# Performance work log

Measured on AMD Instinct MI355X. Metric: run time of the kernel, lower is better.

Reference implementation:

```python
import jax, jax.numpy as jnp
import numpy as np

B, T, C, H = 4, 4096, 1024, 64  # batch, seq, n_embd, head_size

def setup_inputs() -> dict:
    key = jax.random.key(0)
    kx, kq, kk, kv = jax.random.split(key, 4)
    x = jax.random.normal(kx, (B, T, C), dtype=jnp.float32)
    s = 1.0 / np.sqrt(C)
    Wq = jax.random.normal(kq, (C, H), dtype=jnp.float32) * s
    Wk = jax.random.normal(kk, (C, H), dtype=jnp.float32) * s
    Wv = jax.random.normal(kv, (C, H), dtype=jnp.float32) * s
    return {"x": x, "Wq": Wq, "Wk": Wk, "Wv": Wv}

def reference(x, Wq, Wk, Wv):
    B_, T_, C_ = x.shape
    q = x @ Wq  # [B,T,H]
    k = x @ Wk
    v = x @ Wv
    # NOTE: original scales by C**-0.5 (n_embd), not head_size**-0.5
    scale = jnp.asarray(C_, x.dtype) ** -0.5
    wei = jnp.einsum('bth,bsh->bts', q, k) * scale  # [B,T,T]
    causal = jnp.tril(jnp.ones((T_, T_), dtype=bool))
    wei = jnp.where(causal, wei, -jnp.inf)
    wei = jax.nn.softmax(wei, axis=-1)
    out = jnp.einsum('bts,bsh->bth', wei, v)  # [B,T,H]
    return out
```

## Files before the change

### kernel.cpp

```cpp
#include <hip/hip_runtime.h>
#include <hip/hip_bf16.h>
#include <math.h>

#define BB 4
#define TT 4096
#define CC 1024
#define HH 64

typedef __attribute__((ext_vector_type(8))) short short8;
typedef __attribute__((ext_vector_type(8))) unsigned short ushort8;
typedef __attribute__((ext_vector_type(4))) float f32x4;
typedef __attribute__((ext_vector_type(2))) unsigned int uint2v;
typedef __attribute__((ext_vector_type(4))) unsigned int uint4v;

__device__ inline unsigned short f2bf(float f) {
    unsigned int u = __builtin_bit_cast(unsigned int, f);
    unsigned int r = u + 0x7fffu + ((u >> 16) & 1u);
    return (unsigned short)(r >> 16);
}

__device__ inline unsigned int cvtpk(float lo, float hi) {
    unsigned int r;
    asm("v_cvt_pk_bf16_f32 %0, %1, %2" : "=v"(r) : "v"(lo), "v"(hi));
    return r;
}

__device__ inline void gll16(const void* g, void* l) {
    __builtin_amdgcn_global_load_lds(
        (const __attribute__((address_space(1))) unsigned int*)g,
        (__attribute__((address_space(3))) unsigned int*)l,
        16, 0, 0);
}

__device__ inline int soff_strip(int qs) {
    if (qs < 128) return (qs - 64) * 2;
    if (qs < 192) return 128 + (qs - 128) * 3;
    return 320 + (qs - 192) * 4;
}

__global__ __launch_bounds__(256) void wtrans_kernel(
    const float* __restrict__ Wq,
    const float* __restrict__ Wk,
    const float* __restrict__ Wv,
    unsigned short* __restrict__ Wf)
{
    const int t = blockIdx.x * 256 + threadIdx.x;
    const int lane = t & 63;
    const int ntl  = (t >> 6) % 12;
    const int kt   = t / 768;
    const int quad = lane >> 4, n = lane & 15;
    const int m    = ntl >> 2;
    const int col  = (ntl & 3) * 16 + n;
    const float* src = (m == 0) ? Wq : (m == 1) ? Wk : Wv;
    ushort8 u;
#pragma unroll
    for (int j = 0; j < 8; ++j)
        u[j] = f2bf(src[(kt * 32 + quad * 8 + j) * 64 + col]);
    *(ushort8*)(Wf + (size_t)t * 8) = u;
}

__global__ __launch_bounds__(512, 2) void qkv_gemm(
    const float* __restrict__ x,
    const unsigned short* __restrict__ Wf,
    unsigned short* __restrict__ Qb,
    unsigned short* __restrict__ Kf,
    unsigned short* __restrict__ Vf)
{
    __shared__ __align__(16) unsigned char smem[81920];
    float (*Tl)[200] = (float (*)[200])smem;

    const int tid  = threadIdx.x;
    const int lane = tid & 63;
    const int wave = tid >> 6;
    const int n    = lane & 15;
    const int quad = lane >> 4;
    const int mt   = wave & 3;
    const int ch   = wave >> 2;

    const int row0g = blockIdx.x * 64;
    const int b     = row0g >> 12;
    const int st    = (row0g & (TT - 1)) >> 6;

    const char* xg = (const char*)(x + (size_t)row0g * CC);
    const char* wg = (const char*)Wf;

    f32x4 acc[6];
#pragma unroll
    for (int i = 0; i < 6; ++i) acc[i] = (f32x4){0.f, 0.f, 0.f, 0.f};

    auto stage = [&](int bb, int s) {
        unsigned char* base = smem + bb * 40960;
#pragma unroll
        for (int i = 0; i < 2; ++i) {
            const int rr = (i * 8 + wave) * 4 + (lane >> 4);
            const int cb = ((lane & 15) * 16) ^ ((rr & 7) << 4);
            gll16(xg + (size_t)rr * 4096 + s * 256 + cb,
                  base + (i * 8 + wave) * 1024);
        }
#pragma unroll
        for (int i = 0; i < 3; ++i) {
            const int off = (i * 8 + wave) * 1024;
            gll16(wg + (size_t)s * 24576 + off + lane * 16,
                  base + 16384 + off);
        }
    };

    auto compute = [&](int bb) {
        const unsigned char* xb = smem + bb * 40960;
        const unsigned char* wb = xb + 16384;
        const int row = mt * 16 + n;
        const int swz = (n & 7) << 4;
#pragma unroll
        for (int ktl = 0; ktl < 2; ++ktl) {
            const int c0 = (ktl * 128 + quad * 32) ^ swz;
            const int c1 = (ktl * 128 + quad * 32 + 16) ^ swz;
            const float4 f0 = *(const float4*)(xb + row * 256 + c0);
            const float4 f1 = *(const float4*)(xb + row * 256 + c1);
            uint4v u;
            u[0] = cvtpk(f0.x, f0.y);
            u[1] = cvtpk(f0.z, f0.w);
            u[2] = cvtpk(f1.x, f1.y);
            u[3] = cvtpk(f1.z, f1.w);
            const short8 a0 = __builtin_bit_cast(short8, u);
#pragma unroll
            for (int t = 0; t < 6; ++t) {
                const int g = ch * 6 + t;
                const short8 bwv = *(const short8*)(wb + (ktl * 12 + g) * 1024 + lane * 16);
                acc[t] = __builtin_amdgcn_mfma_f32_16x16x32_bf16(a0, bwv, acc[t], 0, 0, 0);
            }
        }
    };

    stage(0, 0);
    __syncthreads();
#pragma unroll 2
    for (int s = 0; s < 16; ++s) {
        if (s + 1 < 16) stage((s + 1) & 1, s + 1);
        compute(s & 1);
        __syncthreads();
    }

#pragma unroll
    for (int t = 0; t < 6; ++t) {
        const int g   = ch * 6 + t;
        const int col = (g >> 2) * 64 + (g & 3) * 16 + n;
#pragma unroll
        for (int r = 0; r < 4; ++r)
            Tl[mt * 16 + quad * 4 + r][col] = acc[t][r];
    }
    __syncthreads();

    {
        const int row = tid & 63;
        const int c0  = (tid >> 6) * 8;
        uint4v w4;
        w4[0] = cvtpk(Tl[row][c0]     * 0.03125f, Tl[row][c0 + 1] * 0.03125f);
        w4[1] = cvtpk(Tl[row][c0 + 2] * 0.03125f, Tl[row][c0 + 3] * 0.03125f);
        w4[2] = cvtpk(Tl[row][c0 + 4] * 0.03125f, Tl[row][c0 + 5] * 0.03125f);
        w4[3] = cvtpk(Tl[row][c0 + 6] * 0.03125f, Tl[row][c0 + 7] * 0.03125f);
        *(uint4v*)(Qb + (size_t)(row0g + row) * HH + c0) = w4;
    }
    {
        const int mt2 = wave >> 1, kk = wave & 1;
        ushort8 u;
#pragma unroll
        for (int j = 0; j < 8; ++j)
            u[j] = f2bf(Tl[mt2 * 16 + n][64 + kk * 32 + quad * 8 + j]);
        const size_t r = (size_t)(((b * 64 + st) * 4 + mt2) * 2 + kk) * 64 + lane;
        *(ushort8*)(Kf + r * 8) = u;
    }
    {
        const int ht = wave >> 1, kv = wave & 1;
        ushort8 u;
#pragma unroll
        for (int j = 0; j < 8; ++j)
            u[j] = f2bf(Tl[kv * 32 + quad * 8 + j][128 + ht * 16 + n]);
        const size_t r = (size_t)(((b * 64 + st) * 4 + ht) * 2 + kv) * 64 + lane;
        *(ushort8*)(Vf + r * 8) = u;
    }
}

__global__ __launch_bounds__(256) void attn_kernel(
    const unsigned short* __restrict__ Qb,
    const unsigned short* __restrict__ Kf,
    const unsigned short* __restrict__ Vf,
    float* __restrict__ out,
    float* __restrict__ scr)
{
    __shared__ unsigned short Ps[4][2][16][72];

    const int tid  = threadIdx.x;
    const int lane = tid & 63;
    const int wave = tid >> 6;
    const int n    = lane & 15;
    const int quad = lane >> 4;

    const int wid = blockIdx.x * 4 + wave;
    const int b   = wid / 640;
    const int u   = wid - b * 640;

    int qs, ci;
    if (u < 64)        { qs = u;                  ci = 0; }
    else if (u < 192)  { const int v = u - 64;  qs = 64  + (v >> 1); ci = v & 1; }
    else if (u < 384)  { const int v = u - 192; const int d = v / 3;
                         qs = 128 + d;            ci = v - 3 * d; }
    else               { const int v = u - 384; qs = 192 + (v >> 2); ci = v & 3; }

    const int stmax = qs >> 2;
    const int st0   = ci << 4;
    const int stEnd = min(stmax, st0 + 15);
    const int nc    = (stmax + 16) >> 4;
    const int qrow  = qs * 16 + n;

    const unsigned short* qp = Qb + ((size_t)b * TT + qrow) * HH;
    const short8 bQ0 = *(const short8*)(qp + quad * 8);
    const short8 bQ1 = *(const short8*)(qp + 32 + quad * 8);

    const unsigned short* KfB = Kf + (size_t)b * 262144;
    const unsigned short* VfB = Vf + (size_t)b * 262144;

    f32x4 O[4];
#pragma unroll
    for (int ht = 0; ht < 4; ++ht) O[ht] = (f32x4){0.f, 0.f, 0.f, 0.f};
    float l = 0.f;

    short8 kA[4], kB[4];
#pragma unroll
    for (int mt = 0; mt < 4; ++mt) {
        const unsigned short* kp = KfB + (size_t)((st0 * 4 + mt) * 2) * 512 + lane * 8;
        kA[mt] = *(const short8*)(kp);
        kB[mt] = *(const short8*)(kp + 512);
    }

    for (int st = st0; st <= stEnd; ++st) {
        f32x4 S[4];
#pragma unroll
        for (int mt = 0; mt < 4; ++mt) {
            f32x4 acc = (f32x4){0.f, 0.f, 0.f, 0.f};
            acc = __builtin_amdgcn_mfma_f32_16x16x32_bf16(kA[mt], bQ0, acc, 0, 0, 0);
            acc = __builtin_amdgcn_mfma_f32_16x16x32_bf16(kB[mt], bQ1, acc, 0, 0, 0);
            S[mt] = acc;
        }

        short8 vA[4], vB[4];
#pragma unroll
        for (int ht = 0; ht < 4; ++ht) {
            const unsigned short* vp = VfB + (size_t)((st * 4 + ht) * 2) * 512 + lane * 8;
            vA[ht] = *(const short8*)(vp);
            vB[ht] = *(const short8*)(vp + 512);
        }
        if (st < stEnd) {
#pragma unroll
            for (int mt = 0; mt < 4; ++mt) {
                const unsigned short* kp = KfB + (size_t)(((st + 1) * 4 + mt) * 2) * 512 + lane * 8;
                kA[mt] = *(const short8*)(kp);
                kB[mt] = *(const short8*)(kp + 512);
            }
        }

        if (st == stmax) {
#pragma unroll
            for (int mt = 0; mt < 4; ++mt) {
                const int sg = st * 64 + mt * 16 + quad * 4;
#pragma unroll
                for (int r = 0; r < 4; ++r)
                    if (sg + r > qrow) S[mt][r] = -INFINITY;
            }
        }

#pragma unroll
        for (int mt = 0; mt < 4; ++mt)
#pragma unroll
            for (int r = 0; r < 4; ++r) {
                const float p = __expf(fminf(S[mt][r], 30.f));
                S[mt][r] = p;
                l += p;
            }

        const int pp = st & 1;
#pragma unroll
        for (int mt = 0; mt < 4; ++mt) {
            uint2v w;
            w[0] = (unsigned int)f2bf(S[mt][0]) | ((unsigned int)f2bf(S[mt][1]) << 16);
            w[1] = (unsigned int)f2bf(S[mt][2]) | ((unsigned int)f2bf(S[mt][3]) << 16);
            *(uint2v*)&Ps[wave][pp][n][mt * 16 + quad * 4] = w;
        }
        asm volatile("s_waitcnt lgkmcnt(0)" ::: "memory");
        const short8 bP0 = *(const short8*)&Ps[wave][pp][n][quad * 8];
        const short8 bP1 = *(const short8*)&Ps[wave][pp][n][32 + quad * 8];

#pragma unroll
        for (int ht = 0; ht < 4; ++ht) {
            O[ht] = __builtin_amdgcn_mfma_f32_16x16x32_bf16(vA[ht], bP0, O[ht], 0, 0, 0);
            O[ht] = __builtin_amdgcn_mfma_f32_16x16x32_bf16(vB[ht], bP1, O[ht], 0, 0, 0);
        }
    }

    l += __shfl_xor(l, 16);
    l += __shfl_xor(l, 32);

    if (nc == 1) {
        const float inv = 1.0f / l;
        float* op = out + ((size_t)b * TT + qrow) * HH;
#pragma unroll
        for (int ht = 0; ht < 4; ++ht) {
            float4 o4;
            o4.x = O[ht][0] * inv;
            o4.y = O[ht][1] * inv;
            o4.z = O[ht][2] * inv;
            o4.w = O[ht][3] * inv;
            *(float4*)(op + ht * 16 + quad * 4) = o4;
        }
    } else {
        float* sb = scr + (size_t)(b * 576 + soff_strip(qs) + ci) * 1040;
        float* rp = sb + n * 64;
#pragma unroll
        for (int ht = 0; ht < 4; ++ht)
            *(f32x4*)(rp + ht * 16 + quad * 4) = O[ht];
        if (quad == 0) sb[1024 + n] = l;
    }
}

__global__ __launch_bounds__(64) void combine_kernel(
    const float* __restrict__ scr,
    float* __restrict__ out)
{
    const int b  = blockIdx.x / 192;
    const int qs = 64 + blockIdx.x % 192;
    const int nc = ((qs >> 2) + 16) >> 4;
    const int base = b * 576 + soff_strip(qs);

    const int t    = threadIdx.x;
    const int row  = t >> 2;
    const int col0 = (t & 3) * 16;

    f32x4 s0 = (f32x4){0.f,0.f,0.f,0.f}, s1 = s0, s2 = s0, s3 = s0;
    float lsum = 0.f;
    for (int ci = 0; ci < nc; ++ci) {
        const float* sb = scr + (size_t)(base + ci) * 1040;
        lsum += sb[1024 + row];
        const float* p = sb + row * 64 + col0;
        s0 += *(const f32x4*)(p);
        s1 += *(const f32x4*)(p + 4);
        s2 += *(const f32x4*)(p + 8);
        s3 += *(const f32x4*)(p + 12);
    }
    const float inv = 1.0f / lsum;
    float* op = out + ((size_t)b * TT + qs * 16 + row) * HH + col0;
    *(f32x4*)(op)      = s0 * inv;
    *(f32x4*)(op + 4)  = s1 * inv;
    *(f32x4*)(op + 8)  = s2 * inv;
    *(f32x4*)(op + 12) = s3 * inv;
}

extern "C" void kernel_launch(void* const* d_in, const int* in_sizes, int n_in,
                              void* d_out, int out_size, void* d_ws, size_t ws_size,
                              hipStream_t stream)
{
    const float* x  = (const float*)d_in[0];
    const float* Wq = (const float*)d_in[1];
    const float* Wk = (const float*)d_in[2];
    const float* Wv = (const float*)d_in[3];

    unsigned short* Qb = (unsigned short*)d_ws;
    unsigned short* Wf = Qb + (size_t)BB * TT * HH;
    unsigned short* Kf = Wf + (size_t)192 * 1024;
    unsigned short* Vf = Kf + (size_t)BB * 262144;
    float*          scr = (float*)(Vf + (size_t)BB * 262144);
    float* out = (float*)d_out;

    wtrans_kernel<<<96, 256, 0, stream>>>(Wq, Wk, Wv, Wf);
    qkv_gemm<<<BB * TT / 64, 512, 0, stream>>>(x, Wf, Qb, Kf, Vf);
    attn_kernel<<<640, 256, 0, stream>>>(Qb, Kf, Vf, out, scr);
    combine_kernel<<<768, 64, 0, stream>>>(scr, out);
}
```

Measured before the change: 150.0 us.

## Process two query strips per wave to reuse K/V fragments

```diff
diff --git a/kernel.cpp b/kernel.cpp
--- a/kernel.cpp
+++ b/kernel.cpp
@@ -180,14 +180,14 @@
     }
 }
 
-__global__ __launch_bounds__(256) void attn_kernel(
+__global__ __launch_bounds__(256, 2) void attn_kernel(
     const unsigned short* __restrict__ Qb,
     const unsigned short* __restrict__ Kf,
     const unsigned short* __restrict__ Vf,
     float* __restrict__ out,
     float* __restrict__ scr)
 {
-    __shared__ unsigned short Ps[4][2][16][72];
+    __shared__ unsigned short Ps[4][2][2][16][72];
 
     const int tid  = threadIdx.x;
     const int lane = tid & 63;
@@ -196,33 +196,41 @@
     const int quad = lane >> 4;
 
     const int wid = blockIdx.x * 4 + wave;
-    const int b   = wid / 640;
-    const int u   = wid - b * 640;
-
-    int qs, ci;
-    if (u < 64)        { qs = u;                  ci = 0; }
-    else if (u < 192)  { const int v = u - 64;  qs = 64  + (v >> 1); ci = v & 1; }
-    else if (u < 384)  { const int v = u - 192; const int d = v / 3;
-                         qs = 128 + d;            ci = v - 3 * d; }
-    else               { const int v = u - 384; qs = 192 + (v >> 2); ci = v & 3; }
-
-    const int stmax = qs >> 2;
+    const int b   = wid / 320;
+    const int u   = wid - b * 320;
+
+    int g, ci;
+    if (u < 32)        { g = u;                 ci = 0; }
+    else if (u < 96)   { const int v = u - 32;  g = 32 + (v >> 1); ci = v & 1; }
+    else if (u < 192)  { const int v = u - 96;  const int d = v / 3;
+                         g = 64 + d;            ci = v - 3 * d; }
+    else               { const int v = u - 192; g = 96 + (v >> 2); ci = v & 3; }
+
+    const int qs0   = 2 * g, qs1 = 2 * g + 1;
+    const int stmax = g >> 1;
     const int st0   = ci << 4;
     const int stEnd = min(stmax, st0 + 15);
     const int nc    = (stmax + 16) >> 4;
-    const int qrow  = qs * 16 + n;
-
-    const unsigned short* qp = Qb + ((size_t)b * TT + qrow) * HH;
-    const short8 bQ0 = *(const short8*)(qp + quad * 8);
-    const short8 bQ1 = *(const short8*)(qp + 32 + quad * 8);
+    const int qrow0 = qs0 * 16 + n;
+    const int qrow1 = qrow0 + 16;
+
+    const unsigned short* qp0 = Qb + ((size_t)b * TT + qrow0) * HH;
+    const unsigned short* qp1 = Qb + ((size_t)b * TT + qrow1) * HH;
+    const short8 bQ0a = *(const short8*)(qp0 + quad * 8);
+    const short8 bQ1a = *(const short8*)(qp0 + 32 + quad * 8);
+    const short8 bQ0b = *(const short8*)(qp1 + quad * 8);
+    const short8 bQ1b = *(const short8*)(qp1 + 32 + quad * 8);
 
     const unsigned short* KfB = Kf + (size_t)b * 262144;
     const unsigned short* VfB = Vf + (size_t)b * 262144;
 
-    f32x4 O[4];
-#pragma unroll
-    for (int ht = 0; ht < 4; ++ht) O[ht] = (f32x4){0.f, 0.f, 0.f, 0.f};
-    float l = 0.f;
+    f32x4 Oa[4], Ob[4];
+#pragma unroll
+    for (int ht = 0; ht < 4; ++ht) {
+        Oa[ht] = (f32x4){0.f, 0.f, 0.f, 0.f};
+        Ob[ht] = (f32x4){0.f, 0.f, 0.f, 0.f};
+    }
+    float la = 0.f, lb = 0.f;
 
     short8 kA[4], kB[4];
 #pragma unroll
@@ -233,13 +241,17 @@
     }
 
     for (int st = st0; st <= stEnd; ++st) {
-        f32x4 S[4];
+        f32x4 Sa[4], Sb[4];
 #pragma unroll
         for (int mt = 0; mt < 4; ++mt) {
-            f32x4 acc = (f32x4){0.f, 0.f, 0.f, 0.f};
-            acc = __builtin_amdgcn_mfma_f32_16x16x32_bf16(kA[mt], bQ0, acc, 0, 0, 0);
-            acc = __builtin_amdgcn_mfma_f32_16x16x32_bf16(kB[mt], bQ1, acc, 0, 0, 0);
-            S[mt] = acc;
+            f32x4 a = (f32x4){0.f, 0.f, 0.f, 0.f};
+            a = __builtin_amdgcn_mfma_f32_16x16x32_bf16(kA[mt], bQ0a, a, 0, 0, 0);
+            a = __builtin_amdgcn_mfma_f32_16x16x32_bf16(kB[mt], bQ1a, a, 0, 0, 0);
+            Sa[mt] = a;
+            f32x4 c = (f32x4){0.f, 0.f, 0.f, 0.f};
+            c = __builtin_amdgcn_mfma_f32_16x16x32_bf16(kA[mt], bQ0b, c, 0, 0, 0);
+            c = __builtin_amdgcn_mfma_f32_16x16x32_bf16(kB[mt], bQ1b, c, 0, 0, 0);
+            Sb[mt] = c;
         }
 
         short8 vA[4], vB[4];
@@ -263,8 +275,10 @@
             for (int mt = 0; mt < 4; ++mt) {
                 const int sg = st * 64 + mt * 16 + quad * 4;
 #pragma unroll
-                for (int r = 0; r < 4; ++r)
-                    if (sg + r > qrow) S[mt][r] = -INFINITY;
+                for (int r = 0; r < 4; ++r) {
+                    if (sg + r > qrow0) Sa[mt][r] = -INFINITY;
+                    if (sg + r > qrow1) Sb[mt][r] = -INFINITY;
+                }
             }
         }
 
@@ -272,52 +286,75 @@
         for (int mt = 0; mt < 4; ++mt)
 #pragma unroll
             for (int r = 0; r < 4; ++r) {
-                const float p = __expf(fminf(S[mt][r], 30.f));
-                S[mt][r] = p;
-                l += p;
+                const float pa = __expf(fminf(Sa[mt][r], 30.f));
+                Sa[mt][r] = pa;
+                la += pa;
+                const float pb = __expf(fminf(Sb[mt][r], 30.f));
+                Sb[mt][r] = pb;
+                lb += pb;
             }
 
         const int pp = st & 1;
 #pragma unroll
         for (int mt = 0; mt < 4; ++mt) {
-            uint2v w;
-            w[0] = (unsigned int)f2bf(S[mt][0]) | ((unsigned int)f2bf(S[mt][1]) << 16);
-            w[1] = (unsigned int)f2bf(S[mt][2]) | ((unsigned int)f2bf(S[mt][3]) << 16);
-            *(uint2v*)&Ps[wave][pp][n][mt * 16 + quad * 4] = w;
+            uint2v wa, wb2;
+            wa[0]  = (unsigned int)f2bf(Sa[mt][0]) | ((unsigned int)f2bf(Sa[mt][1]) << 16);
+            wa[1]  = (unsigned int)f2bf(Sa[mt][2]) | ((unsigned int)f2bf(Sa[mt][3]) << 16);
+            wb2[0] = (unsigned int)f2bf(Sb[mt][0]) | ((unsigned int)f2bf(Sb[mt][1]) << 16);
+            wb2[1] = (unsigned int)f2bf(Sb[mt][2]) | ((unsigned int)f2bf(Sb[mt][3]) << 16);
+            *(uint2v*)&Ps[wave][0][pp][n][mt * 16 + quad * 4] = wa;
+            *(uint2v*)&Ps[wave][1][pp][n][mt * 16 + quad * 4] = wb2;
         }
         asm volatile("s_waitcnt lgkmcnt(0)" ::: "memory");
-        const short8 bP0 = *(const short8*)&Ps[wave][pp][n][quad * 8];
-        const short8 bP1 = *(const short8*)&Ps[wave][pp][n][32 + quad * 8];
+        const short8 bP0a = *(const short8*)&Ps[wave][0][pp][n][quad * 8];
+        const short8 bP1a = *(const short8*)&Ps[wave][0][pp][n][32 + quad * 8];
+        const short8 bP0b = *(const short8*)&Ps[wave][1][pp][n][quad * 8];
+        const short8 bP1b = *(const short8*)&Ps[wave][1][pp][n][32 + quad * 8];
 
 #pragma unroll
         for (int ht = 0; ht < 4; ++ht) {
-            O[ht] = __builtin_amdgcn_mfma_f32_16x16x32_bf16(vA[ht], bP0, O[ht], 0, 0, 0);
-            O[ht] = __builtin_amdgcn_mfma_f32_16x16x32_bf16(vB[ht], bP1, O[ht], 0, 0, 0);
-        }
-    }
-
-    l += __shfl_xor(l, 16);
-    l += __shfl_xor(l, 32);
+            Oa[ht] = __builtin_amdgcn_mfma_f32_16x16x32_bf16(vA[ht], bP0a, Oa[ht], 0, 0, 0);
+            Oa[ht] = __builtin_amdgcn_mfma_f32_16x16x32_bf16(vB[ht], bP1a, Oa[ht], 0, 0, 0);
+            Ob[ht] = __builtin_amdgcn_mfma_f32_16x16x32_bf16(vA[ht], bP0b, Ob[ht], 0, 0, 0);
+            Ob[ht] = __builtin_amdgcn_mfma_f32_16x16x32_bf16(vB[ht], bP1b, Ob[ht], 0, 0, 0);
+        }
+    }
+
+    la += __shfl_xor(la, 16);
+    la += __shfl_xor(la, 32);
+    lb += __shfl_xor(lb, 16);
+    lb += __shfl_xor(lb, 32);
 
     if (nc == 1) {
-        const float inv = 1.0f / l;
-        float* op = out + ((size_t)b * TT + qrow) * HH;
+        const float inva = 1.0f / la;
+        const float invb = 1.0f / lb;
+        float* op0 = out + ((size_t)b * TT + qrow0) * HH;
+        float* op1 = out + ((size_t)b * TT + qrow1) * HH;
 #pragma unroll
         for (int ht = 0; ht < 4; ++ht) {
             float4 o4;
-            o4.x = O[ht][0] * inv;
-            o4.y = O[ht][1] * inv;
-            o4.z = O[ht][2] * inv;
-            o4.w = O[ht][3] * inv;
-            *(float4*)(op + ht * 16 + quad * 4) = o4;
+            o4.x = Oa[ht][0] * inva; o4.y = Oa[ht][1] * inva;
+            o4.z = Oa[ht][2] * inva; o4.w = Oa[ht][3] * inva;
+            *(float4*)(op0 + ht * 16 + quad * 4) = o4;
+            float4 o5;
+            o5.x = Ob[ht][0] * invb; o5.y = Ob[ht][1] * invb;
+            o5.z = Ob[ht][2] * invb; o5.w = Ob[ht][3] * invb;
+            *(float4*)(op1 + ht * 16 + quad * 4) = o5;
         }
     } else {
-        float* sb = scr + (size_t)(b * 576 + soff_strip(qs) + ci) * 1040;
-        float* rp = sb + n * 64;
-#pragma unroll
-        for (int ht = 0; ht < 4; ++ht)
-            *(f32x4*)(rp + ht * 16 + quad * 4) = O[ht];
-        if (quad == 0) sb[1024 + n] = l;
+        float* sb0 = scr + (size_t)(b * 576 + soff_strip(qs0) + ci) * 1040;
+        float* sb1 = scr + (size_t)(b * 576 + soff_strip(qs1) + ci) * 1040;
+        float* rp0 = sb0 + n * 64;
+        float* rp1 = sb1 + n * 64;
+#pragma unroll
+        for (int ht = 0; ht < 4; ++ht) {
+            *(f32x4*)(rp0 + ht * 16 + quad * 4) = Oa[ht];
+            *(f32x4*)(rp1 + ht * 16 + quad * 4) = Ob[ht];
+        }
+        if (quad == 0) {
+            sb0[1024 + n] = la;
+            sb1[1024 + n] = lb;
+        }
     }
 }
 
@@ -371,6 +408,6 @@
 
     wtrans_kernel<<<96, 256, 0, stream>>>(Wq, Wk, Wv, Wf);
     qkv_gemm<<<BB * TT / 64, 512, 0, stream>>>(x, Wf, Qb, Kf, Vf);
-    attn_kernel<<<640, 256, 0, stream>>>(Qb, Kf, Vf, out, scr);
+    attn_kernel<<<320, 256, 0, stream>>>(Qb, Kf, Vf, out, scr);
     combine_kernel<<<768, 64, 0, stream>>>(scr, out);
 }
```

Measured after the change: 152.5 us. No clear change (+1.7%).
